# Optimization experiments

Measured on AMD Instinct MI355X. Metric: run time of the kernel, lower is better.

## Reference

```python
import jax, jax.numpy as jnp
import numpy as np

TWO_PI = np.float32(2.0 * np.pi)


def setup_inputs() -> dict:
    H, W = 2048, 2048
    MAX_COC = 21  # gain_params['max_CoC']
    key = jax.random.key(0)
    k1, k2 = jax.random.split(key)
    image = jax.random.uniform(k1, (H, W, 3), dtype=jnp.float32)
    # per-pixel circle-of-confusion kernel size (what GetSparseTensor derives from the depth map)
    kernel_size_flatten = jax.random.randint(k2, (H * W,), 0, MAX_COC + 1, dtype=jnp.int32)
    return {"image": image, "kernel_size_flatten": kernel_size_flatten, "max_coc": MAX_COC}


def reference(image, kernel_size_flatten, max_coc):
    """Spatially-variant Gaussian defocus blur.

    Faithful to CudaGetDefocusWeightsKernel: each input pixel px with
    kernel_size k > 1 scatters image[px] * N(offset; sigma=k/6) to all
    in-bounds neighbors within k//2; pixels with k <= 1 pass through
    (weight 1.0 at themselves). Out-of-bounds targets are skipped (the
    kernel clamps the loop range), realized here by a discarded padding
    ring on the output buffer.
    """
    H, W, C = image.shape
    half_max = max_coc // 2  # static Python int

    ks = kernel_size_flatten.reshape(H, W)            # [H, W] int
    half_k = (ks // 2).astype(jnp.float32)            # kernel_size // 2
    blur = ks > 1                                     # [H, W] bool
    sigma = ks.astype(jnp.float32) / 6.0
    sigma_safe = jnp.where(blur, sigma, 1.0)          # avoid 0-div on identity pixels
    inv_2s2 = 0.5 / (sigma_safe * sigma_safe)         # [H, W]
    norm = 1.0 / (TWO_PI * sigma_safe * sigma_safe)   # [H, W]

    offs = jnp.arange(-half_max, half_max + 1)
    dys, dxs = jnp.meshgrid(offs, offs, indexing="ij")
    dys, dxs = dys.reshape(-1), dxs.reshape(-1)       # [K^2] scatter offsets

    pad = half_max
    out0 = jnp.zeros((H + 2 * pad, W + 2 * pad, C), image.dtype)

    def step(out, off):
        dy, dx = off
        d2 = (dy * dy + dx * dx).astype(jnp.float32)
        in_win = (jnp.abs(dy).astype(jnp.float32) <= half_k) & (
            jnp.abs(dx).astype(jnp.float32) <= half_k
        )
        gw = jnp.exp(-d2 * inv_2s2) * norm            # [H, W] Gaussian weight
        wmap = jnp.where(blur & in_win, gw, 0.0)
        wmap = jnp.where((~blur) & (dy == 0) & (dx == 0), 1.0, wmap)
        contrib = image * wmap[..., None]             # [H, W, C]
        y0, x0 = pad + dy, pad + dx
        cur = jax.lax.dynamic_slice(out, (y0, x0, 0), (H, W, C))
        out = jax.lax.dynamic_update_slice(out, cur + contrib, (y0, x0, 0))
        return out, None

    out, _ = jax.lax.scan(step, out0, (dys, dxs))
    return out[pad:pad + H, pad:pad + W, :]
```

## Files before the change

### kernel.cpp

```cpp
#include <hip/hip_runtime.h>
#include <hip/hip_fp16.h>

#define IMG_W 2048
#define IMG_H 2048
#define HALF  10
#define TILE  64
#define LW 84
#define NSTG (LW * LW)

#define L_KSD 51
#define L_KSB 204
#define L_NDW (22 * L_KSD)

__device__ __forceinline__ __half2 h2(uint u)  { union { uint a; __half2 b; } c; c.a = u; return c.b; }
__device__ __forceinline__ uint pack2(float a, float b) {
    return (uint)__half_as_ushort(__float2half(a)) |
           ((uint)__half_as_ushort(__float2half(b)) << 16);
}
__device__ __forceinline__ float wyv(int k, int oy) {
    int a = abs(oy), hk = k >> 1;
    if (a > hk) return 0.f;
    if (k <= 1) return 1.f;
    float kk = (float)(k * k);
    return expf(-(float)(oy * oy) * 18.f / kk) * 5.7295780f / kk;
}
__device__ __forceinline__ float wxv(int k, int ox) {
    int a = abs(ox), hk = k >> 1;
    if (a > hk) return 0.f;
    if (k <= 1) return 1.f;
    float kk = (float)(k * k);
    return expf(-(float)(ox * ox) * 18.f / kk);
}

#define FMA_LO(acc, px, w) \
    asm("v_pk_fma_f16 %0, %1, %2, %0 op_sel:[0,0,0] op_sel_hi:[0,1,1]" \
        : "+v"(acc) : "v"(px), "v"(w))
#define FMA_HI(acc, px, w) \
    asm("v_pk_fma_f16 %0, %1, %2, %0 op_sel:[1,0,0] op_sel_hi:[1,1,1]" \
        : "+v"(acc) : "v"(px), "v"(w))
#define MUL_WYLO(d, wx2, wy2) \
    asm("v_pk_mul_f16 %0, %1, %2 op_sel:[0,0] op_sel_hi:[1,0]" \
        : "=v"(d) : "v"(wx2), "v"(wy2))
#define MUL_WYHI(d, wx2, wy2) \
    asm("v_pk_mul_f16 %0, %1, %2 op_sel:[0,1] op_sel_hi:[1,1]" \
        : "=v"(d) : "v"(wx2), "v"(wy2))

__global__ __launch_bounds__(512, 4)
void defocus_pipe_kernel(const float* __restrict__ img,
                         const int* __restrict__ ks,
                         float* __restrict__ out)
{
    __shared__ uint  lutw[L_NDW + 2];
    __shared__ uint2 tile[NSTG];

    const int tid = threadIdx.x;
    const int X0 = blockIdx.x * TILE;
    const int Y0 = blockIdx.y * TILE;

    for (int i = tid; i < L_NDW; i += 512) {
        int k = i / L_KSD;
        int d = i - k * L_KSD;
        float lo = 0.f, hi = 0.f;
        if (d < 22) {
            lo = wyv(k, d - 10);
            hi = wyv(k, d - 11);
        } else if (d < 36) {
            int j = d - 22;
            lo = wxv(k, 2 * j - 13);
            hi = wxv(k, 2 * j - 12);
        } else if (d < 50) {
            int j = d - 36;
            lo = wxv(k, 2 * j - 12);
            hi = wxv(k, 2 * j - 11);
        }
        lutw[i] = pack2(lo, hi);
    }

    for (int i = tid; i < NSTG; i += 512) {
        int r = i / LW;
        int c = i - r * LW;
        int gy = Y0 - HALF + r;
        int gx = X0 - HALF + c;
        float fr = 0.f, fg = 0.f, fb = 0.f;
        uint koffB = 0;
        if (gy >= 0 && gy < IMG_H && gx >= 0 && gx < IMG_W) {
            int p = gy * IMG_W + gx;
            fr = img[p * 3 + 0];
            fg = img[p * 3 + 1];
            fb = img[p * 3 + 2];
            koffB = (uint)(ks[p] * L_KSB);
        }
        uint2 v;
        v.x = pack2(fr, fg);
        v.y = koffB | ((uint)__half_as_ushort(__float2half(fb)) << 16);
        tile[r * LW + (c & 3) * 21 + (c >> 2)] = v;
    }
    __syncthreads();

    const int tx = tid & 15;
    const int ty = tid >> 4;
    const int colbase = tx * 4;
    const int rowbase = ty * 2;
    const int pxbase  = rowbase * LW + tx;

    uint A32[2][3] = {{0,0,0},{0,0,0}}, A10[2][3] = {{0,0,0},{0,0,0}};
    float mc[2][4][3];
    #pragma unroll
    for (int r = 0; r < 2; ++r)
        #pragma unroll
        for (int c = 0; c < 3; ++c)
            mc[r][0][c] = mc[r][1][c] = mc[r][2][c] = mc[r][3][c] = 0.f;

#define PIDX(b) (((b) & 3) * 21 + ((b) >> 2))

#define PXG(buf, B0)                                   \
    { buf[0] = tile[pxrow + PIDX((B0) + 0)];           \
      buf[1] = tile[pxrow + PIDX((B0) + 1)];           \
      buf[2] = tile[pxrow + PIDX((B0) + 2)];           \
      buf[3] = tile[pxrow + PIDX((B0) + 3)];           \
      buf[4] = tile[pxrow + PIDX((B0) + 4)];           \
      buf[5] = tile[pxrow + PIDX((B0) + 5)];           \
      buf[6] = tile[pxrow + PIDX((B0) + 6)];           \
      buf[7] = tile[pxrow + PIDX((B0) + 7)]; }

#define WLD1(w, pvv, aa, b)                                                        \
    { const uint* wp = (const uint*)((const char*)lutw + ((pvv).y & 0xffffu));     \
      (w).x = wp[(aa)];                                                            \
      (w).y = (((b) & 1) == 0) ? wp[22 + ((b) >> 1)] : wp[36 + (((b) - 1) >> 1)];  \
      (w).z = (((b) & 1) == 0) ? wp[23 + ((b) >> 1)] : wp[37 + (((b) - 1) >> 1)]; }

#define WG(wv, buf, aa, B0)                 \
    { WLD1(wv[0], buf[0], aa, (B0) + 0);    \
      WLD1(wv[1], buf[1], aa, (B0) + 1);    \
      WLD1(wv[2], buf[2], aa, (B0) + 2);    \
      WLD1(wv[3], buf[3], aa, (B0) + 3);    \
      WLD1(wv[4], buf[4], aa, (B0) + 4);    \
      WLD1(wv[5], buf[5], aa, (B0) + 5);    \
      WLD1(wv[6], buf[6], aa, (B0) + 6);    \
      WLD1(wv[7], buf[7], aa, (B0) + 7); }

#define FMA1(pvv, w)                                                   \
    { uint W320, W100, W321, W101;                                     \
      MUL_WYLO(W320, (w).y, (w).x); MUL_WYLO(W100, (w).z, (w).x);      \
      MUL_WYHI(W321, (w).y, (w).x); MUL_WYHI(W101, (w).z, (w).x);      \
      FMA_LO(A32[0][0], (pvv).x, W320);                                \
      FMA_HI(A32[0][1], (pvv).x, W320);                                \
      FMA_HI(A32[0][2], (pvv).y, W320);                                \
      FMA_LO(A10[0][0], (pvv).x, W100);                                \
      FMA_HI(A10[0][1], (pvv).x, W100);                                \
      FMA_HI(A10[0][2], (pvv).y, W100);                                \
      FMA_LO(A32[1][0], (pvv).x, W321);                                \
      FMA_HI(A32[1][1], (pvv).x, W321);                                \
      FMA_HI(A32[1][2], (pvv).y, W321);                                \
      FMA_LO(A10[1][0], (pvv).x, W101);                                \
      FMA_HI(A10[1][1], (pvv).x, W101);                                \
      FMA_HI(A10[1][2], (pvv).y, W101); }

#define FMAG(buf, wv)          \
    { FMA1(buf[0], wv[0]);     \
      FMA1(buf[1], wv[1]);     \
      FMA1(buf[2], wv[2]);     \
      FMA1(buf[3], wv[3]);     \
      FMA1(buf[4], wv[4]);     \
      FMA1(buf[5], wv[5]);     \
      FMA1(buf[6], wv[6]);     \
      FMA1(buf[7], wv[7]); }

#define ROW(aa)                            \
    { const int pxrow = pxbase + (aa) * LW;\
      uint2 p0[8], p1[8];                  \
      uint3 wv[8];                         \
      PXG(p0, 0);                          \
      PXG(p1, 8);                          \
      WG(wv, p0, (aa), 0);                 \
      FMAG(p0, wv);                        \
      PXG(p0, 16);                         \
      WG(wv, p1, (aa), 8);                 \
      FMAG(p1, wv);                        \
      WG(wv, p0, (aa), 16);                \
      FMAG(p0, wv); }

#define FLUSH()                                                        \
    { _Pragma("unroll")                                                \
      for (int r = 0; r < 2; ++r) {                                    \
          _Pragma("unroll")                                            \
          for (int c = 0; c < 3; ++c) {                                \
              float2 f3 = __half22float2(h2(A32[r][c]));               \
              float2 f1 = __half22float2(h2(A10[r][c]));               \
              mc[r][3][c] += f3.x; mc[r][2][c] += f3.y;                \
              mc[r][1][c] += f1.x; mc[r][0][c] += f1.y;                \
              A32[r][c] = 0; A10[r][c] = 0;                            \
          }                                                            \
      } }

    #pragma unroll 1
    for (int ap = 0; ap < 11; ++ap) {
        ROW(2 * ap);
        ROW(2 * ap + 1);
        FLUSH();
    }

    #pragma unroll
    for (int r = 0; r < 2; ++r) {
        int gy = Y0 + rowbase + r;
        #pragma unroll
        for (int m = 0; m < 4; ++m) {
            int gx = X0 + colbase + m;
            int o = (gy * IMG_W + gx) * 3;
            out[o + 0] = mc[r][m][0];
            out[o + 1] = mc[r][m][1];
            out[o + 2] = mc[r][m][2];
        }
    }
#undef ROW
#undef FLUSH
#undef PXG
#undef WG
#undef FMAG
#undef FMA1
#undef WLD1
#undef PIDX
}

extern "C" void kernel_launch(void* const* d_in, const int* in_sizes, int n_in,
                              void* d_out, int out_size, void* d_ws, size_t ws_size,
                              hipStream_t stream) {
    const float* img = (const float*)d_in[0];
    const int*   ks  = (const int*)d_in[1];
    float* out = (float*)d_out;

    dim3 grid(IMG_W / TILE, IMG_H / TILE);
    dim3 block(512);
    defocus_pipe_kernel<<<grid, block, 0, stream>>>(img, ks, out);
}
```

Baseline: 176.8 us.

## Register-block four output rows per thread with 256-thread blocks

Each thread now accumulates a 4x4 output patch instead of 2x4, sweeping 24 input rows instead of 22. The weight LUT gets two extra vertical entries per kernel size, and the block shrinks to 256 threads. The aim is to reuse each LDS pixel load and weight lookup across more output rows, which cuts shared-memory traffic per output. In exchange, accumulator register pressure roughly doubles, which may limit occupancy, and the padded tile row stride changes the LDS layout.

```diff
diff --git a/kernel.cpp b/kernel.cpp
--- a/kernel.cpp
+++ b/kernel.cpp
@@ -5,11 +5,11 @@
 #define IMG_H 2048
 #define HALF  10
 #define TILE  64
-#define LW 84
-#define NSTG (LW * LW)
-
-#define L_KSD 51
-#define L_KSB 204
+#define HLO   84
+#define SLOTS 86
+
+#define L_KSD 55
+#define L_KSB 220
 #define L_NDW (22 * L_KSD)
 
 __device__ __forceinline__ __half2 h2(uint u)  { union { uint a; __half2 b; } c; c.a = u; return c.b; }
@@ -32,12 +32,12 @@
     return expf(-(float)(ox * ox) * 18.f / kk);
 }
 
-#define FMA_LO(acc, px, w) \
+#define FMA_LO(acc, px, wgt) \
     asm("v_pk_fma_f16 %0, %1, %2, %0 op_sel:[0,0,0] op_sel_hi:[0,1,1]" \
-        : "+v"(acc) : "v"(px), "v"(w))
-#define FMA_HI(acc, px, w) \
+        : "+v"(acc) : "v"(px), "v"(wgt))
+#define FMA_HI(acc, px, wgt) \
     asm("v_pk_fma_f16 %0, %1, %2, %0 op_sel:[1,0,0] op_sel_hi:[1,1,1]" \
-        : "+v"(acc) : "v"(px), "v"(w))
+        : "+v"(acc) : "v"(px), "v"(wgt))
 #define MUL_WYLO(d, wx2, wy2) \
     asm("v_pk_mul_f16 %0, %1, %2 op_sel:[0,0] op_sel_hi:[1,0]" \
         : "=v"(d) : "v"(wx2), "v"(wy2))
@@ -45,40 +45,40 @@
     asm("v_pk_mul_f16 %0, %1, %2 op_sel:[0,1] op_sel_hi:[1,1]" \
         : "=v"(d) : "v"(wx2), "v"(wy2))
 
-__global__ __launch_bounds__(512, 4)
-void defocus_pipe_kernel(const float* __restrict__ img,
-                         const int* __restrict__ ks,
-                         float* __restrict__ out)
+__global__ __launch_bounds__(256, 2)
+void defocus_44b_kernel(const float* __restrict__ img,
+                        const int* __restrict__ ks,
+                        float* __restrict__ out)
 {
     __shared__ uint  lutw[L_NDW + 2];
-    __shared__ uint2 tile[NSTG];
+    __shared__ uint2 tile[HLO * SLOTS];
 
     const int tid = threadIdx.x;
     const int X0 = blockIdx.x * TILE;
     const int Y0 = blockIdx.y * TILE;
 
-    for (int i = tid; i < L_NDW; i += 512) {
+    for (int i = tid; i < L_NDW; i += 256) {
         int k = i / L_KSD;
         int d = i - k * L_KSD;
         float lo = 0.f, hi = 0.f;
-        if (d < 22) {
-            lo = wyv(k, d - 10);
-            hi = wyv(k, d - 11);
-        } else if (d < 36) {
-            int j = d - 22;
+        if (d < 26) {
+            lo = wyv(k, d - 12);
+            hi = wyv(k, d - 13);
+        } else if (d < 40) {
+            int j = d - 26;
             lo = wxv(k, 2 * j - 13);
             hi = wxv(k, 2 * j - 12);
-        } else if (d < 50) {
-            int j = d - 36;
+        } else if (d < 54) {
+            int j = d - 40;
             lo = wxv(k, 2 * j - 12);
             hi = wxv(k, 2 * j - 11);
         }
         lutw[i] = pack2(lo, hi);
     }
 
-    for (int i = tid; i < NSTG; i += 512) {
-        int r = i / LW;
-        int c = i - r * LW;
+    for (int i = tid; i < HLO * HLO; i += 256) {
+        int r = i / HLO;
+        int c = i - r * HLO;
         int gy = Y0 - HALF + r;
         int gx = X0 - HALF + c;
         float fr = 0.f, fg = 0.f, fb = 0.f;
@@ -93,20 +93,20 @@
         uint2 v;
         v.x = pack2(fr, fg);
         v.y = koffB | ((uint)__half_as_ushort(__float2half(fb)) << 16);
-        tile[r * LW + (c & 3) * 21 + (c >> 2)] = v;
+        tile[r * SLOTS + (c & 3) * 21 + (c >> 2)] = v;
     }
     __syncthreads();
 
     const int tx = tid & 15;
     const int ty = tid >> 4;
     const int colbase = tx * 4;
-    const int rowbase = ty * 2;
-    const int pxbase  = rowbase * LW + tx;
-
-    uint A32[2][3] = {{0,0,0},{0,0,0}}, A10[2][3] = {{0,0,0},{0,0,0}};
-    float mc[2][4][3];
+    const int rowbase = ty * 4;
+    const int pxbase  = rowbase * SLOTS + tx;
+
+    uint A32[4][3] = {}, A10[4][3] = {};
+    float mc[4][4][3];
     #pragma unroll
-    for (int r = 0; r < 2; ++r)
+    for (int r = 0; r < 4; ++r)
         #pragma unroll
         for (int c = 0; c < 3; ++c)
             mc[r][0][c] = mc[r][1][c] = mc[r][2][c] = mc[r][3][c] = 0.f;
@@ -123,11 +123,12 @@
       buf[6] = tile[pxrow + PIDX((B0) + 6)];           \
       buf[7] = tile[pxrow + PIDX((B0) + 7)]; }
 
-#define WLD1(w, pvv, aa, b)                                                        \
+#define WLD1(q, pvv, aa, b)                                                        \
     { const uint* wp = (const uint*)((const char*)lutw + ((pvv).y & 0xffffu));     \
-      (w).x = wp[(aa)];                                                            \
-      (w).y = (((b) & 1) == 0) ? wp[22 + ((b) >> 1)] : wp[36 + (((b) - 1) >> 1)];  \
-      (w).z = (((b) & 1) == 0) ? wp[23 + ((b) >> 1)] : wp[37 + (((b) - 1) >> 1)]; }
+      (q).x = wp[(aa) + 2];                                                        \
+      (q).y = wp[(aa)];                                                            \
+      (q).z = (((b) & 1) == 0) ? wp[26 + ((b) >> 1)] : wp[40 + (((b) - 1) >> 1)];  \
+      (q).w = (((b) & 1) == 0) ? wp[27 + ((b) >> 1)] : wp[41 + (((b) - 1) >> 1)]; }
 
 #define WG(wv, buf, aa, B0)                 \
     { WLD1(wv[0], buf[0], aa, (B0) + 0);    \
@@ -139,22 +140,21 @@
       WLD1(wv[6], buf[6], aa, (B0) + 6);    \
       WLD1(wv[7], buf[7], aa, (B0) + 7); }
 
-#define FMA1(pvv, w)                                                   \
-    { uint W320, W100, W321, W101;                                     \
-      MUL_WYLO(W320, (w).y, (w).x); MUL_WYLO(W100, (w).z, (w).x);      \
-      MUL_WYHI(W321, (w).y, (w).x); MUL_WYHI(W101, (w).z, (w).x);      \
-      FMA_LO(A32[0][0], (pvv).x, W320);                                \
-      FMA_HI(A32[0][1], (pvv).x, W320);                                \
-      FMA_HI(A32[0][2], (pvv).y, W320);                                \
-      FMA_LO(A10[0][0], (pvv).x, W100);                                \
-      FMA_HI(A10[0][1], (pvv).x, W100);                                \
-      FMA_HI(A10[0][2], (pvv).y, W100);                                \
-      FMA_LO(A32[1][0], (pvv).x, W321);                                \
-      FMA_HI(A32[1][1], (pvv).x, W321);                                \
-      FMA_HI(A32[1][2], (pvv).y, W321);                                \
-      FMA_LO(A10[1][0], (pvv).x, W101);                                \
-      FMA_HI(A10[1][1], (pvv).x, W101);                                \
-      FMA_HI(A10[1][2], (pvv).y, W101); }
+#define FMA1(pvv, q)                                                   \
+    { uint Wr[4], Vr[4];                                               \
+      MUL_WYLO(Wr[0], (q).z, (q).x); MUL_WYHI(Wr[1], (q).z, (q).x);    \
+      MUL_WYLO(Wr[2], (q).z, (q).y); MUL_WYHI(Wr[3], (q).z, (q).y);    \
+      MUL_WYLO(Vr[0], (q).w, (q).x); MUL_WYHI(Vr[1], (q).w, (q).x);    \
+      MUL_WYLO(Vr[2], (q).w, (q).y); MUL_WYHI(Vr[3], (q).w, (q).y);    \
+      _Pragma("unroll")                                                \
+      for (int r = 0; r < 4; ++r) {                                    \
+          FMA_LO(A32[r][0], (pvv).x, Wr[r]);                           \
+          FMA_HI(A32[r][1], (pvv).x, Wr[r]);                           \
+          FMA_HI(A32[r][2], (pvv).y, Wr[r]);                           \
+          FMA_LO(A10[r][0], (pvv).x, Vr[r]);                           \
+          FMA_HI(A10[r][1], (pvv).x, Vr[r]);                           \
+          FMA_HI(A10[r][2], (pvv).y, Vr[r]);                           \
+      } }
 
 #define FMAG(buf, wv)          \
     { FMA1(buf[0], wv[0]);     \
@@ -166,23 +166,23 @@
       FMA1(buf[6], wv[6]);     \
       FMA1(buf[7], wv[7]); }
 
-#define ROW(aa)                            \
-    { const int pxrow = pxbase + (aa) * LW;\
-      uint2 p0[8], p1[8];                  \
-      uint3 wv[8];                         \
-      PXG(p0, 0);                          \
-      PXG(p1, 8);                          \
-      WG(wv, p0, (aa), 0);                 \
-      FMAG(p0, wv);                        \
-      PXG(p0, 16);                         \
-      WG(wv, p1, (aa), 8);                 \
-      FMAG(p1, wv);                        \
-      WG(wv, p0, (aa), 16);                \
+#define ROW(aa)                                \
+    { const int pxrow = pxbase + (aa) * SLOTS; \
+      uint2 p0[8], p1[8];                      \
+      uint4 wv[8];                             \
+      PXG(p0, 0);                              \
+      PXG(p1, 8);                              \
+      WG(wv, p0, (aa), 0);                     \
+      FMAG(p0, wv);                            \
+      PXG(p0, 16);                             \
+      WG(wv, p1, (aa), 8);                     \
+      FMAG(p1, wv);                            \
+      WG(wv, p0, (aa), 16);                    \
       FMAG(p0, wv); }
 
 #define FLUSH()                                                        \
     { _Pragma("unroll")                                                \
-      for (int r = 0; r < 2; ++r) {                                    \
+      for (int r = 0; r < 4; ++r) {                                    \
           _Pragma("unroll")                                            \
           for (int c = 0; c < 3; ++c) {                                \
               float2 f3 = __half22float2(h2(A32[r][c]));               \
@@ -194,14 +194,14 @@
       } }
 
     #pragma unroll 1
-    for (int ap = 0; ap < 11; ++ap) {
+    for (int ap = 0; ap < 12; ++ap) {
         ROW(2 * ap);
         ROW(2 * ap + 1);
         FLUSH();
     }
 
     #pragma unroll
-    for (int r = 0; r < 2; ++r) {
+    for (int r = 0; r < 4; ++r) {
         int gy = Y0 + rowbase + r;
         #pragma unroll
         for (int m = 0; m < 4; ++m) {
@@ -230,6 +230,6 @@
     float* out = (float*)d_out;
 
     dim3 grid(IMG_W / TILE, IMG_H / TILE);
-    dim3 block(512);
-    defocus_pipe_kernel<<<grid, block, 0, stream>>>(img, ks, out);
-}
+    dim3 block(256);
+    defocus_44b_kernel<<<grid, block, 0, stream>>>(img, ks, out);
+}
```

New measurement: 201.2 us. +13.8%, slower.

## Move Gaussian weight LUT from shared memory to global workspace built by separate kernel

Applied to the files above, without the earlier changes.

The per-block construction of the weight lookup table in LDS is removed. A small separate kernel now builds a transposed LUT (rows by offset, columns by kernel size) in the workspace buffer, and the main kernel reads weights through global loads, which should mostly hit cache. This drops redundant per-block expf work and frees LDS, but turns the hot-loop weight loads from LDS reads into global/cache loads with higher latency and divergent addresses, and it adds a second kernel launch.

```diff
diff --git a/kernel.cpp b/kernel.cpp
--- a/kernel.cpp
+++ b/kernel.cpp
@@ -8,9 +8,10 @@
 #define LW 84
 #define NSTG (LW * LW)
 
-#define L_KSD 51
-#define L_KSB 204
-#define L_NDW (22 * L_KSD)
+#define LROWS 50
+#define LRSB  128
+#define LUT_BYTES (LROWS * LRSB)
+#define LMID  3200
 
 __device__ __forceinline__ __half2 h2(uint u)  { union { uint a; __half2 b; } c; c.a = u; return c.b; }
 __device__ __forceinline__ uint pack2(float a, float b) {
@@ -32,12 +33,34 @@
     return expf(-(float)(ox * ox) * 18.f / kk);
 }
 
-#define FMA_LO(acc, px, w) \
+__global__ void build_lut_kernel(uint* __restrict__ lutg)
+{
+    int i = blockIdx.x * blockDim.x + threadIdx.x;
+    if (i >= LROWS * 22) return;
+    int row = i / 22;
+    int k   = i - row * 22;
+    float lo = 0.f, hi = 0.f;
+    if (row < 22) {
+        lo = wyv(k, row - 10);
+        hi = wyv(k, row - 11);
+    } else if (row < 36) {
+        int j = row - 22;
+        lo = wxv(k, 2 * j - 13);
+        hi = wxv(k, 2 * j - 12);
+    } else {
+        int j = row - 36;
+        lo = wxv(k, 2 * j - 12);
+        hi = wxv(k, 2 * j - 11);
+    }
+    lutg[row * (LRSB / 4) + k] = pack2(lo, hi);
+}
+
+#define FMA_LO(acc, px, wgt) \
     asm("v_pk_fma_f16 %0, %1, %2, %0 op_sel:[0,0,0] op_sel_hi:[0,1,1]" \
-        : "+v"(acc) : "v"(px), "v"(w))
-#define FMA_HI(acc, px, w) \
+        : "+v"(acc) : "v"(px), "v"(wgt))
+#define FMA_HI(acc, px, wgt) \
     asm("v_pk_fma_f16 %0, %1, %2, %0 op_sel:[1,0,0] op_sel_hi:[1,1,1]" \
-        : "+v"(acc) : "v"(px), "v"(w))
+        : "+v"(acc) : "v"(px), "v"(wgt))
 #define MUL_WYLO(d, wx2, wy2) \
     asm("v_pk_mul_f16 %0, %1, %2 op_sel:[0,0] op_sel_hi:[1,0]" \
         : "=v"(d) : "v"(wx2), "v"(wy2))
@@ -46,35 +69,16 @@
         : "=v"(d) : "v"(wx2), "v"(wy2))
 
 __global__ __launch_bounds__(512, 4)
-void defocus_pipe_kernel(const float* __restrict__ img,
+void defocus_glut_kernel(const float* __restrict__ img,
                          const int* __restrict__ ks,
+                         const char* __restrict__ lutmid,
                          float* __restrict__ out)
 {
-    __shared__ uint  lutw[L_NDW + 2];
     __shared__ uint2 tile[NSTG];
 
     const int tid = threadIdx.x;
     const int X0 = blockIdx.x * TILE;
     const int Y0 = blockIdx.y * TILE;
-
-    for (int i = tid; i < L_NDW; i += 512) {
-        int k = i / L_KSD;
-        int d = i - k * L_KSD;
-        float lo = 0.f, hi = 0.f;
-        if (d < 22) {
-            lo = wyv(k, d - 10);
-            hi = wyv(k, d - 11);
-        } else if (d < 36) {
-            int j = d - 22;
-            lo = wxv(k, 2 * j - 13);
-            hi = wxv(k, 2 * j - 12);
-        } else if (d < 50) {
-            int j = d - 36;
-            lo = wxv(k, 2 * j - 12);
-            hi = wxv(k, 2 * j - 11);
-        }
-        lutw[i] = pack2(lo, hi);
-    }
 
     for (int i = tid; i < NSTG; i += 512) {
         int r = i / LW;
@@ -82,17 +86,17 @@
         int gy = Y0 - HALF + r;
         int gx = X0 - HALF + c;
         float fr = 0.f, fg = 0.f, fb = 0.f;
-        uint koffB = 0;
+        uint koff = 0;
         if (gy >= 0 && gy < IMG_H && gx >= 0 && gx < IMG_W) {
             int p = gy * IMG_W + gx;
             fr = img[p * 3 + 0];
             fg = img[p * 3 + 1];
             fb = img[p * 3 + 2];
-            koffB = (uint)(ks[p] * L_KSB);
+            koff = (uint)(ks[p] * 4);
         }
         uint2 v;
         v.x = pack2(fr, fg);
-        v.y = koffB | ((uint)__half_as_ushort(__float2half(fb)) << 16);
+        v.y = koff | ((uint)__half_as_ushort(__float2half(fb)) << 16);
         tile[r * LW + (c & 3) * 21 + (c >> 2)] = v;
     }
     __syncthreads();
@@ -112,6 +116,7 @@
             mc[r][0][c] = mc[r][1][c] = mc[r][2][c] = mc[r][3][c] = 0.f;
 
 #define PIDX(b) (((b) & 3) * 21 + ((b) >> 2))
+#define WROW(r) ((r) * LRSB - LMID)
 
 #define PXG(buf, B0)                                   \
     { buf[0] = tile[pxrow + PIDX((B0) + 0)];           \
@@ -123,11 +128,13 @@
       buf[6] = tile[pxrow + PIDX((B0) + 6)];           \
       buf[7] = tile[pxrow + PIDX((B0) + 7)]; }
 
-#define WLD1(w, pvv, aa, b)                                                        \
-    { const uint* wp = (const uint*)((const char*)lutw + ((pvv).y & 0xffffu));     \
-      (w).x = wp[(aa)];                                                            \
-      (w).y = (((b) & 1) == 0) ? wp[22 + ((b) >> 1)] : wp[36 + (((b) - 1) >> 1)];  \
-      (w).z = (((b) & 1) == 0) ? wp[23 + ((b) >> 1)] : wp[37 + (((b) - 1) >> 1)]; }
+#define WLD1(q, pvv, aa, b)                                                        \
+    { const char* wb = lutmid + ((pvv).y & 0xffffu);                               \
+      (q).x = *(const uint*)(wb + WROW(aa));                                       \
+      (q).y = (((b) & 1) == 0) ? *(const uint*)(wb + WROW(22 + ((b) >> 1)))        \
+                               : *(const uint*)(wb + WROW(36 + (((b) - 1) >> 1))); \
+      (q).z = (((b) & 1) == 0) ? *(const uint*)(wb + WROW(23 + ((b) >> 1)))        \
+                               : *(const uint*)(wb + WROW(37 + (((b) - 1) >> 1))); }
 
 #define WG(wv, buf, aa, B0)                 \
     { WLD1(wv[0], buf[0], aa, (B0) + 0);    \
@@ -139,10 +146,10 @@
       WLD1(wv[6], buf[6], aa, (B0) + 6);    \
       WLD1(wv[7], buf[7], aa, (B0) + 7); }
 
-#define FMA1(pvv, w)                                                   \
+#define FMA1(pvv, q)                                                   \
     { uint W320, W100, W321, W101;                                     \
-      MUL_WYLO(W320, (w).y, (w).x); MUL_WYLO(W100, (w).z, (w).x);      \
-      MUL_WYHI(W321, (w).y, (w).x); MUL_WYHI(W101, (w).z, (w).x);      \
+      MUL_WYLO(W320, (q).y, (q).x); MUL_WYLO(W100, (q).z, (q).x);      \
+      MUL_WYHI(W321, (q).y, (q).x); MUL_WYHI(W101, (q).z, (q).x);      \
       FMA_LO(A32[0][0], (pvv).x, W320);                                \
       FMA_HI(A32[0][1], (pvv).x, W320);                                \
       FMA_HI(A32[0][2], (pvv).y, W320);                                \
@@ -219,6 +226,7 @@
 #undef FMAG
 #undef FMA1
 #undef WLD1
+#undef WROW
 #undef PIDX
 }
 
@@ -228,8 +236,12 @@
     const float* img = (const float*)d_in[0];
     const int*   ks  = (const int*)d_in[1];
     float* out = (float*)d_out;
+    uint*  lutg = (uint*)d_ws;
+
+    build_lut_kernel<<<(LROWS * 22 + 255) / 256, 256, 0, stream>>>(lutg);
 
     dim3 grid(IMG_W / TILE, IMG_H / TILE);
     dim3 block(512);
-    defocus_pipe_kernel<<<grid, block, 0, stream>>>(img, ks, out);
-}
+    defocus_glut_kernel<<<grid, block, 0, stream>>>(
+        img, ks, (const char*)d_ws + LMID, out);
+}
```

Result: slower. 373.6 us (+111.3%).
